# Optimization experiments

Hardware: AMD Instinct MI355X
Metric: run time of the kernel (lower is better)

## Reference

```python
import jax, jax.numpy as jnp
import numpy as np

N_NODES = 100000
N_EDGES = 1600000
N_GRAPHS = 128
K_HOPS = 3  # TAGConv default K
HIDDEN = 128
IN_FEAT = 4
NUM_CLASSES = 2


def setup_inputs() -> dict:
    key = jax.random.key(0)
    ks = jax.random.split(key, 10)
    x = jax.random.normal(ks[0], (N_NODES, IN_FEAT), dtype=jnp.float32)
    W1 = jax.random.normal(ks[1], (K_HOPS + 1, IN_FEAT, HIDDEN), dtype=jnp.float32) * 0.1
    b1 = jax.random.normal(ks[2], (HIDDEN,), dtype=jnp.float32) * 0.1
    W2 = jax.random.normal(ks[3], (K_HOPS + 1, HIDDEN, HIDDEN), dtype=jnp.float32) * 0.1
    b2 = jax.random.normal(ks[4], (HIDDEN,), dtype=jnp.float32) * 0.1
    Wlin = jax.random.normal(ks[5], (HIDDEN, NUM_CLASSES), dtype=jnp.float32) * 0.1
    blin = jax.random.normal(ks[6], (NUM_CLASSES,), dtype=jnp.float32) * 0.1
    edge_index = jax.random.randint(ks[7], (2, N_EDGES), 0, N_NODES, dtype=jnp.int32)
    batch = jnp.sort(jax.random.randint(ks[8], (N_NODES,), 0, N_GRAPHS, dtype=jnp.int32))
    return {"x": x, "W1": W1, "b1": b1, "W2": W2, "b2": b2,
            "Wlin": Wlin, "blin": blin, "edge_index": edge_index, "batch": batch}


def _gcn_norm(edge_index, num_nodes):
    # symmetric normalization, no self-loops (TAGConv: add_self_loops=False)
    row, col = edge_index[0], edge_index[1]
    ones = jnp.ones((edge_index.shape[1],), dtype=jnp.float32)
    deg = jax.ops.segment_sum(ones, col, num_segments=num_nodes)
    dinv = jnp.where(deg > 0, jax.lax.rsqrt(jnp.maximum(deg, 1.0)), 0.0)
    return dinv[row] * dinv[col]  # [E]


def _tagconv(x, row, col, norm, W, b):
    # out = sum_k (A_norm^k x) @ W[k] + b
    out = x @ W[0]
    h = x
    for k in range(1, W.shape[0]):
        h = jax.ops.segment_sum(h[row] * norm[:, None], col, num_segments=x.shape[0])
        out = out + h @ W[k]
    return out + b


def reference(x, W1, b1, W2, b2, Wlin, blin, edge_index, batch):
    row, col = edge_index[0], edge_index[1]
    norm = _gcn_norm(edge_index, x.shape[0])
    h = jax.nn.relu(_tagconv(x, row, col, norm, W1, b1))
    h = jax.nn.relu(_tagconv(h, row, col, norm, W2, b2))
    # global mean pool over graphs
    sums = jax.ops.segment_sum(h, batch, num_segments=N_GRAPHS)
    cnts = jax.ops.segment_sum(jnp.ones((h.shape[0],), dtype=h.dtype), batch, num_segments=N_GRAPHS)
    pooled = sums / jnp.maximum(cnts, 1.0)[:, None]
    # dropout is identity in eval mode
    logits = pooled @ Wlin + blin
    return jax.nn.softmax(logits, axis=-1)
```

## Files before the change

### kernel.cpp

```cpp
#include <hip/hip_runtime.h>

#define NNODES 100000
#define NEDGES 1600000
#define NGRAPHS 128
#define HID 128
#define NBKT 782
#define CHUNK 8192
#define NCHB ((NEDGES + CHUNK - 1) / CHUNK)
#define MAXB 3072

typedef unsigned short ushort_t;
typedef unsigned int uint_t;
typedef __attribute__((ext_vector_type(8))) short short8;
typedef __attribute__((ext_vector_type(4))) float floatx4;

__device__ __forceinline__ float bf2f(ushort_t u) {
    return __uint_as_float(((unsigned)u) << 16);
}
__device__ __forceinline__ ushort_t f2bf(float f) {
    unsigned u = __float_as_uint(f);
    return (ushort_t)((u + 0x7fffu + ((u >> 16) & 1u)) >> 16);
}

__global__ void hist_k(const int* __restrict__ col, int* __restrict__ bcnt) {
    __shared__ int l[NBKT];
    for (int i = threadIdx.x; i < NBKT; i += 256) l[i] = 0;
    __syncthreads();
    int base = blockIdx.x * CHUNK;
    int lim = base + CHUNK < NEDGES ? base + CHUNK : NEDGES;
    for (int e = base + threadIdx.x; e < lim; e += 256)
        atomicAdd(&l[col[e] >> 7], 1);
    __syncthreads();
    for (int i = threadIdx.x; i < NBKT; i += 256)
        if (l[i]) atomicAdd(&bcnt[i], l[i]);
}

__global__ void bscan_k(const int* __restrict__ bcnt, int* __restrict__ bbase,
                        int* __restrict__ gc) {
    __shared__ int l[1024];
    int t = threadIdx.x;
    int v0 = (t < NBKT) ? bcnt[t] : 0;
    l[t] = v0;
    __syncthreads();
    for (int d = 1; d < 1024; d <<= 1) {
        int v = (t >= d) ? l[t - d] : 0;
        __syncthreads();
        l[t] += v;
        __syncthreads();
    }
    if (t < NBKT) { int ex = l[t] - v0; bbase[t] = ex; gc[t] = ex; }
    if (t == 0) bbase[NBKT] = NEDGES;
}

__global__ void bfill_k(const int* __restrict__ row, const int* __restrict__ col,
                        int* __restrict__ gc, uint_t* __restrict__ entry) {
    __shared__ int lcnt[NBKT], lbase[NBKT];
    for (int i = threadIdx.x; i < NBKT; i += 256) lcnt[i] = 0;
    __syncthreads();
    int base = blockIdx.x * CHUNK;
    int lim = base + CHUNK < NEDGES ? base + CHUNK : NEDGES;
    for (int e = base + threadIdx.x; e < lim; e += 256)
        atomicAdd(&lcnt[col[e] >> 7], 1);
    __syncthreads();
    for (int i = threadIdx.x; i < NBKT; i += 256) {
        int c = lcnt[i];
        lbase[i] = c ? atomicAdd(&gc[i], c) : 0;
        lcnt[i] = 0;
    }
    __syncthreads();
    for (int e = base + threadIdx.x; e < lim; e += 256) {
        int c = col[e];
        int b = c >> 7;
        int pos = lbase[b] + atomicAdd(&lcnt[b], 1);
        entry[pos] = (uint_t)row[e] | ((uint_t)(c & 127) << 17);
    }
}

__global__ void sortb_k(const uint_t* __restrict__ entry, const int* __restrict__ bbase,
                        int* __restrict__ csr_src, int* __restrict__ degi,
                        int* __restrict__ off) {
    __shared__ uint_t ents[MAXB];
    __shared__ uint_t sorted[MAXB];
    __shared__ int ncnt[128], nsc[128], nfill[128];
    int b = blockIdx.x;
    int base = bbase[b];
    int cnt = bbase[b + 1] - base;
    if (cnt > MAXB) cnt = MAXB;
    int t = threadIdx.x;
    if (t < 128) { ncnt[t] = 0; nfill[t] = 0; }
    __syncthreads();
    for (int i = t; i < cnt; i += 256) {
        uint_t v = entry[base + i];
        ents[i] = v;
        atomicAdd(&ncnt[v >> 17], 1);
    }
    __syncthreads();
    if (t < 128) nsc[t] = ncnt[t];
    __syncthreads();
    for (int d = 1; d < 128; d <<= 1) {
        int v = (t >= d && t < 128) ? nsc[t - d] : 0;
        __syncthreads();
        if (t < 128) nsc[t] += v;
        __syncthreads();
    }
    if (t < 128) {
        int n = b * 128 + t;
        if (n < NNODES) { degi[n] = ncnt[t]; off[n] = base + nsc[t]; }
        nsc[t] -= ncnt[t];
    }
    __syncthreads();
    for (int i = t; i < cnt; i += 256) {
        uint_t v = ents[i];
        int dl = v >> 17;
        int pos = nsc[dl] + atomicAdd(&nfill[dl], 1);
        sorted[pos] = v & 0x1FFFFu;
    }
    __syncthreads();
    for (int i = t; i < cnt; i += 256) csr_src[base + i] = (int)sorted[i];
}

__global__ void dinv_kernel(const int* __restrict__ degi, float* __restrict__ dinv) {
    int i = blockIdx.x * blockDim.x + threadIdx.x;
    if (i < NNODES) {
        int d = degi[i];
        dinv[i] = (d > 0) ? rsqrtf((float)d) : 0.0f;
    }
}

__global__ void gprop4(const int* __restrict__ off, const int* __restrict__ csr_src,
                       const float* __restrict__ dinv,
                       const float* __restrict__ hin, float* __restrict__ hout) {
    int n = blockIdx.x * 256 + threadIdx.x;
    if (n >= NNODES) return;
    int k = n ? off[n - 1] : 0;
    int end = off[n];
    float dn = dinv[n];
    float4 acc = {0.f, 0.f, 0.f, 0.f};
    for (; k + 3 < end; k += 4) {
        int s0 = csr_src[k], s1 = csr_src[k + 1], s2 = csr_src[k + 2], s3 = csr_src[k + 3];
        float w0 = dinv[s0] * dn, w1 = dinv[s1] * dn, w2 = dinv[s2] * dn, w3 = dinv[s3] * dn;
        float4 v0 = *(const float4*)(hin + s0 * 4);
        float4 v1 = *(const float4*)(hin + s1 * 4);
        float4 v2 = *(const float4*)(hin + s2 * 4);
        float4 v3 = *(const float4*)(hin + s3 * 4);
        acc.x += w0 * v0.x + w1 * v1.x + w2 * v2.x + w3 * v3.x;
        acc.y += w0 * v0.y + w1 * v1.y + w2 * v2.y + w3 * v3.y;
        acc.z += w0 * v0.z + w1 * v1.z + w2 * v2.z + w3 * v3.z;
        acc.w += w0 * v0.w + w1 * v1.w + w2 * v2.w + w3 * v3.w;
    }
    for (; k < end; k++) {
        int s = csr_src[k];
        float w = dinv[s] * dn;
        float4 v = *(const float4*)(hin + s * 4);
        acc.x += w * v.x; acc.y += w * v.y; acc.z += w * v.z; acc.w += w * v.w;
    }
    *(float4*)(hout + n * 4) = acc;
}

__device__ __forceinline__ void acc8(float* a, float wgt, uint4 v) {
    a[0] += wgt * __uint_as_float(v.x << 16);
    a[1] += wgt * __uint_as_float(v.x & 0xffff0000u);
    a[2] += wgt * __uint_as_float(v.y << 16);
    a[3] += wgt * __uint_as_float(v.y & 0xffff0000u);
    a[4] += wgt * __uint_as_float(v.z << 16);
    a[5] += wgt * __uint_as_float(v.z & 0xffff0000u);
    a[6] += wgt * __uint_as_float(v.w << 16);
    a[7] += wgt * __uint_as_float(v.w & 0xffff0000u);
}

__global__ void gprop128(const int* __restrict__ off, const int* __restrict__ csr_src,
                         const float* __restrict__ dinv,
                         const ushort_t* __restrict__ hin, ushort_t* __restrict__ hout) {
    int t = blockIdx.x * 256 + threadIdx.x;
    int n = t >> 4, lane = t & 15;
    if (n >= NNODES) return;
    int k = n ? off[n - 1] : 0;
    int end = off[n];
    float dn = dinv[n];
    int fo = lane * 8;
    float a[8] = {0.f, 0.f, 0.f, 0.f, 0.f, 0.f, 0.f, 0.f};
    for (; k + 3 < end; k += 4) {
        int s0 = csr_src[k], s1 = csr_src[k + 1], s2 = csr_src[k + 2], s3 = csr_src[k + 3];
        float w0 = dinv[s0] * dn, w1 = dinv[s1] * dn, w2 = dinv[s2] * dn, w3 = dinv[s3] * dn;
        uint4 v0 = *(const uint4*)(hin + s0 * HID + fo);
        uint4 v1 = *(const uint4*)(hin + s1 * HID + fo);
        uint4 v2 = *(const uint4*)(hin + s2 * HID + fo);
        uint4 v3 = *(const uint4*)(hin + s3 * HID + fo);
        acc8(a, w0, v0); acc8(a, w1, v1); acc8(a, w2, v2); acc8(a, w3, v3);
    }
    for (; k < end; k++) {
        int s = csr_src[k];
        float w = dinv[s] * dn;
        uint4 v = *(const uint4*)(hin + s * HID + fo);
        acc8(a, w, v);
    }
    uint4 o;
    o.x = (unsigned)f2bf(a[0]) | ((unsigned)f2bf(a[1]) << 16);
    o.y = (unsigned)f2bf(a[2]) | ((unsigned)f2bf(a[3]) << 16);
    o.z = (unsigned)f2bf(a[4]) | ((unsigned)f2bf(a[5]) << 16);
    o.w = (unsigned)f2bf(a[6]) | ((unsigned)f2bf(a[7]) << 16);
    *(uint4*)(hout + n * HID + fo) = o;
}

__global__ void combine1(const float* __restrict__ x, const float* __restrict__ h1,
                         const float* __restrict__ h2, const float* __restrict__ h3,
                         const float* __restrict__ W1, const float* __restrict__ b1,
                         ushort_t* __restrict__ P0) {
    __shared__ float hs[4][16];
    int n0 = blockIdx.x * 4;
    int j = threadIdx.x;
    if (j < 64) {
        int n = j >> 4, v = j & 15, k = v >> 2, i = v & 3;
        const float* src = (k == 0) ? x : (k == 1) ? h1 : (k == 2) ? h2 : h3;
        hs[n][v] = src[(n0 + n) * 4 + i];
    }
    __syncthreads();
    float w[16];
#pragma unroll
    for (int v = 0; v < 16; v++) w[v] = W1[v * 128 + j];
    float bb = b1[j];
#pragma unroll
    for (int n = 0; n < 4; n++) {
        float acc = bb;
#pragma unroll
        for (int v = 0; v < 16; v++) acc += hs[n][v] * w[v];
        P0[(n0 + n) * 128 + j] = f2bf(fmaxf(acc, 0.0f));
    }
}

__global__ void wt_kernel(const float* __restrict__ W2, ushort_t* __restrict__ Wt) {
    int t = blockIdx.x * 256 + threadIdx.x;
    if (t >= 512 * 128) return;
    int j = t >> 9, k = t & 511;
    Wt[t] = f2bf(W2[k * 128 + j]);
}

__global__ __launch_bounds__(256) void gemm4p(
    const ushort_t* __restrict__ P0, const ushort_t* __restrict__ P1,
    const ushort_t* __restrict__ P2, const ushort_t* __restrict__ P3,
    const ushort_t* __restrict__ Wt, const float* __restrict__ b2,
    const int* __restrict__ batch, float* __restrict__ sums) {
    __shared__ ushort_t Bs[32768];
    int tid = threadIdx.x;
    int w = tid >> 6, lane = tid & 63;
    int r16 = lane & 15, kg = lane >> 4;
    int tb = blockIdx.x * 128 + w * 32;
    bool active = (tb < NNODES);
    floatx4 acc[2][8];
#pragma unroll
    for (int s = 0; s < 2; s++)
#pragma unroll
        for (int n = 0; n < 8; n++) acc[s][n] = (floatx4){0.f, 0.f, 0.f, 0.f};
    const ushort_t* Ps[4] = {P0, P1, P2, P3};
    for (int stage = 0; stage < 2; stage++) {
        __syncthreads();
#pragma unroll
        for (int i = 0; i < 16; i++) {
            int idx = i * 256 + tid;
            int r = idx >> 5;
            int slot = idx & 31;
            int cb = (slot * 16) ^ ((r & 7) << 4);
            *(uint4*)((char*)Bs + r * 512 + cb) =
                *(const uint4*)(Wt + r * 512 + stage * 256 + slot * 8);
        }
        __syncthreads();
        if (active) {
#pragma unroll
            for (int hh = 0; hh < 2; hh++) {
                const ushort_t* P = Ps[stage * 2 + hh];
#pragma unroll
                for (int k0 = 0; k0 < 128; k0 += 32) {
                    int f = k0 + kg * 8;
                    short8 a0 = *(const short8*)(P + (tb + r16) * HID + f);
                    short8 a1 = *(const short8*)(P + (tb + 16 + r16) * HID + f);
#pragma unroll
                    for (int n = 0; n < 8; n++) {
                        int r = n * 16 + r16;
                        int cb = (hh * 256 + k0 * 2 + kg * 16) ^ ((r & 7) << 4);
                        short8 b = *(const short8*)((const char*)Bs + r * 512 + cb);
                        acc[0][n] = __builtin_amdgcn_mfma_f32_16x16x32_bf16(a0, b, acc[0][n], 0, 0, 0);
                        acc[1][n] = __builtin_amdgcn_mfma_f32_16x16x32_bf16(a1, b, acc[1][n], 0, 0, 0);
                    }
                }
            }
        }
    }
    if (!active) return;
    float bb[8];
#pragma unroll
    for (int n = 0; n < 8; n++) bb[n] = b2[n * 16 + r16];
    int g0 = batch[tb], g31 = batch[tb + 31];
    if (g0 == g31) {
#pragma unroll
        for (int n = 0; n < 8; n++) {
            float s = 0.0f;
#pragma unroll
            for (int st = 0; st < 2; st++)
#pragma unroll
                for (int r = 0; r < 4; r++) s += fmaxf(acc[st][n][r] + bb[n], 0.0f);
            s += __shfl_xor(s, 16);
            s += __shfl_xor(s, 32);
            if (kg == 0) atomicAdd(&sums[g0 * HID + n * 16 + r16], s);
        }
    } else {
#pragma unroll
        for (int st = 0; st < 2; st++)
#pragma unroll
            for (int r = 0; r < 4; r++) {
                int g = batch[tb + st * 16 + kg * 4 + r];
#pragma unroll
                for (int n = 0; n < 8; n++)
                    atomicAdd(&sums[g * HID + n * 16 + r16], fmaxf(acc[st][n][r] + bb[n], 0.0f));
            }
    }
}

__global__ void bounds_kernel(const int* __restrict__ batch,
                              int* __restrict__ first, int* __restrict__ last) {
    int n = blockIdx.x * 256 + threadIdx.x;
    if (n >= NNODES) return;
    int g = batch[n];
    if (n == 0 || batch[n - 1] != g) first[g] = n;
    if (n == NNODES - 1 || batch[n + 1] != g) last[g] = n;
}

__global__ void head_kernel(const float* __restrict__ sums, const int* __restrict__ first,
                            const int* __restrict__ last,
                            const float* __restrict__ Wlin, const float* __restrict__ blin,
                            float* __restrict__ out) {
    int g = threadIdx.x;
    if (g >= NGRAPHS) return;
    int f = first[g];
    float cnt = (f >= 0) ? (float)(last[g] - f + 1) : 1.0f;
    float l0 = blin[0], l1 = blin[1];
    for (int i = 0; i < HID; i++) {
        float p = sums[g * HID + i] / cnt;
        l0 += p * Wlin[i * 2 + 0];
        l1 += p * Wlin[i * 2 + 1];
    }
    float m = fmaxf(l0, l1);
    float e0 = __expf(l0 - m), e1 = __expf(l1 - m);
    float s = e0 + e1;
    out[g * 2 + 0] = e0 / s;
    out[g * 2 + 1] = e1 / s;
}

#define NPAD      100096
#define OFF_DINV  0
#define OFF_DEGI  (OFF_DINV + NPAD)
#define OFF_OFF   (OFF_DEGI + NPAD)
#define OFF_BCNT  (OFF_OFF + NPAD)
#define OFF_BBASE (OFF_BCNT + 800)
#define OFF_GC    (OFF_BBASE + 800)
#define OFF_ENT   (OFF_GC + 800)
#define OFF_SRC   (OFF_ENT + NEDGES)
#define OFF_P0    (OFF_SRC + NEDGES)
#define OFF_P1    (OFF_P0 + NNODES * HID / 2)
#define OFF_P2    (OFF_P1 + NNODES * HID / 2)
#define OFF_P3    (OFF_P2 + NNODES * HID / 2)
#define OFF_H1    (OFF_P3 + NNODES * HID / 2)
#define OFF_H2    (OFF_H1 + NNODES * 4)
#define OFF_H3    (OFF_H2 + NNODES * 4)
#define OFF_WT    (OFF_H3 + NNODES * 4)
#define OFF_SUMS  (OFF_WT + 32768)
#define OFF_FIRST (OFF_SUMS + NGRAPHS * HID)
#define OFF_LAST  (OFF_FIRST + NGRAPHS)

extern "C" void kernel_launch(void* const* d_in, const int* in_sizes, int n_in,
                              void* d_out, int out_size, void* d_ws, size_t ws_size,
                              hipStream_t stream) {
    const float* x    = (const float*)d_in[0];
    const float* W1   = (const float*)d_in[1];
    const float* b1   = (const float*)d_in[2];
    const float* W2   = (const float*)d_in[3];
    const float* b2   = (const float*)d_in[4];
    const float* Wlin = (const float*)d_in[5];
    const float* blin = (const float*)d_in[6];
    const int* ei     = (const int*)d_in[7];
    const int* batch  = (const int*)d_in[8];
    float* out = (float*)d_out;

    const int* row = ei;
    const int* col = ei + NEDGES;

    float* ws = (float*)d_ws;
    float* dinv    = ws + OFF_DINV;
    int*   degi    = (int*)(ws + OFF_DEGI);
    int*   off     = (int*)(ws + OFF_OFF);
    int*   bcnt    = (int*)(ws + OFF_BCNT);
    int*   bbase   = (int*)(ws + OFF_BBASE);
    int*   gc      = (int*)(ws + OFF_GC);
    uint_t* ent    = (uint_t*)(ws + OFF_ENT);
    int*   csr_src = (int*)(ws + OFF_SRC);
    ushort_t* P0   = (ushort_t*)(ws + OFF_P0);
    ushort_t* P1   = (ushort_t*)(ws + OFF_P1);
    ushort_t* P2   = (ushort_t*)(ws + OFF_P2);
    ushort_t* P3   = (ushort_t*)(ws + OFF_P3);
    float* h1      = ws + OFF_H1;
    float* h2      = ws + OFF_H2;
    float* h3      = ws + OFF_H3;
    ushort_t* Wt   = (ushort_t*)(ws + OFF_WT);
    float* sums    = ws + OFF_SUMS;
    int*   first   = (int*)(ws + OFF_FIRST);
    int*   last    = (int*)(ws + OFF_LAST);

    hipMemsetAsync(bcnt, 0, 800 * sizeof(int), stream);
    hipMemsetAsync(sums, 0, NGRAPHS * HID * sizeof(float), stream);
    hipMemsetAsync(first, 0xFF, 2 * NGRAPHS * sizeof(int), stream);

    hist_k<<<NCHB, 256, 0, stream>>>(col, bcnt);
    bscan_k<<<1, 1024, 0, stream>>>(bcnt, bbase, gc);
    bfill_k<<<NCHB, 256, 0, stream>>>(row, col, gc, ent);
    sortb_k<<<NBKT, 256, 0, stream>>>(ent, bbase, csr_src, degi, off);
    dinv_kernel<<<(NNODES + 255) / 256, 256, 0, stream>>>(degi, dinv);
    wt_kernel<<<(512 * 128) / 256, 256, 0, stream>>>(W2, Wt);
    bounds_kernel<<<(NNODES + 255) / 256, 256, 0, stream>>>(batch, first, last);

    gprop4<<<(NNODES + 255) / 256, 256, 0, stream>>>(off, csr_src, dinv, x, h1);
    gprop4<<<(NNODES + 255) / 256, 256, 0, stream>>>(off, csr_src, dinv, h1, h2);
    gprop4<<<(NNODES + 255) / 256, 256, 0, stream>>>(off, csr_src, dinv, h2, h3);
    combine1<<<NNODES / 4, 128, 0, stream>>>(x, h1, h2, h3, W1, b1, P0);

    gprop128<<<(NNODES * 16) / 256, 256, 0, stream>>>(off, csr_src, dinv, P0, P1);
    gprop128<<<(NNODES * 16) / 256, 256, 0, stream>>>(off, csr_src, dinv, P1, P2);
    gprop128<<<(NNODES * 16) / 256, 256, 0, stream>>>(off, csr_src, dinv, P2, P3);

    gemm4p<<<(NNODES + 127) / 128, 256, 0, stream>>>(P0, P1, P2, P3, Wt, b2, batch, sums);

    head_kernel<<<1, 128, 0, stream>>>(sums, first, last, Wlin, blin, out);
}
```

Baseline: 360.1 us.

## Degree-sort nodes within buckets for balanced gathers and fuse setup kernels

The sort kernel now builds a per-bucket permutation that orders each 128-node bucket by in-degree (capped at 63). The gather propagation kernels process nodes in that order, so threads in the same wavefront handle nodes of similar degree, which is meant to cut divergence and idle lanes. The dinv, weight-transpose and graph-bounds kernels are merged into one launch, and the three memsets are merged into one contiguous zeroing. In exchange there is an extra indirection load per node, output writes become less sequential within a bucket, and the head now relies on zero-initialised first/last for empty graphs.

```diff
diff --git a/kernel.cpp b/kernel.cpp
--- a/kernel.cpp
+++ b/kernel.cpp
@@ -5,6 +5,7 @@
 #define NGRAPHS 128
 #define HID 128
 #define NBKT 782
+#define NPAD  (NBKT * 128)
 #define CHUNK 8192
 #define NCHB ((NEDGES + CHUNK - 1) / CHUNK)
 #define MAXB 3072
@@ -78,16 +79,18 @@
 
 __global__ void sortb_k(const uint_t* __restrict__ entry, const int* __restrict__ bbase,
                         int* __restrict__ csr_src, int* __restrict__ degi,
-                        int* __restrict__ off) {
+                        int* __restrict__ off, int* __restrict__ perm) {
     __shared__ uint_t ents[MAXB];
     __shared__ uint_t sorted[MAXB];
     __shared__ int ncnt[128], nsc[128], nfill[128];
+    __shared__ int dcnt[64], dbase_s[64], dfill[64];
     int b = blockIdx.x;
     int base = bbase[b];
     int cnt = bbase[b + 1] - base;
     if (cnt > MAXB) cnt = MAXB;
     int t = threadIdx.x;
     if (t < 128) { ncnt[t] = 0; nfill[t] = 0; }
+    if (t >= 128 && t < 192) { dcnt[t - 128] = 0; dfill[t - 128] = 0; }
     __syncthreads();
     for (int i = t; i < cnt; i += 256) {
         uint_t v = entry[base + i];
@@ -103,10 +106,13 @@
         if (t < 128) nsc[t] += v;
         __syncthreads();
     }
+    int mydeg = 0;
     if (t < 128) {
         int n = b * 128 + t;
         if (n < NNODES) { degi[n] = ncnt[t]; off[n] = base + nsc[t]; }
         nsc[t] -= ncnt[t];
+        mydeg = ncnt[t] > 63 ? 63 : ncnt[t];
+        atomicAdd(&dcnt[mydeg], 1);
     }
     __syncthreads();
     for (int i = t; i < cnt; i += 256) {
@@ -115,22 +121,42 @@
         int pos = nsc[dl] + atomicAdd(&nfill[dl], 1);
         sorted[pos] = v & 0x1FFFFu;
     }
-    __syncthreads();
+    if (t == 0) {
+        int run = 0;
+        for (int i = 0; i < 64; i++) { dbase_s[i] = run; run += dcnt[i]; }
+    }
+    __syncthreads();
+    if (t < 128) {
+        int pos = dbase_s[mydeg] + atomicAdd(&dfill[mydeg], 1);
+        perm[b * 128 + pos] = b * 128 + t;
+    }
     for (int i = t; i < cnt; i += 256) csr_src[base + i] = (int)sorted[i];
 }
 
-__global__ void dinv_kernel(const int* __restrict__ degi, float* __restrict__ dinv) {
-    int i = blockIdx.x * blockDim.x + threadIdx.x;
+__global__ void misc_k(const int* __restrict__ degi, float* __restrict__ dinv,
+                       const float* __restrict__ W2, ushort_t* __restrict__ Wt,
+                       const int* __restrict__ batch,
+                       int* __restrict__ first, int* __restrict__ last) {
+    int i = blockIdx.x * 256 + threadIdx.x;
     if (i < NNODES) {
         int d = degi[i];
         dinv[i] = (d > 0) ? rsqrtf((float)d) : 0.0f;
+        int g = batch[i];
+        if (i == 0 || batch[i - 1] != g) first[g] = i;
+        if (i == NNODES - 1 || batch[i + 1] != g) last[g] = i;
+    }
+    if (i < 512 * 128) {
+        int j = i >> 9, k = i & 511;
+        Wt[i] = f2bf(W2[k * 128 + j]);
     }
 }
 
 __global__ void gprop4(const int* __restrict__ off, const int* __restrict__ csr_src,
-                       const float* __restrict__ dinv,
+                       const float* __restrict__ dinv, const int* __restrict__ perm,
                        const float* __restrict__ hin, float* __restrict__ hout) {
-    int n = blockIdx.x * 256 + threadIdx.x;
+    int i = blockIdx.x * 256 + threadIdx.x;
+    if (i >= NPAD) return;
+    int n = perm[i];
     if (n >= NNODES) return;
     int k = n ? off[n - 1] : 0;
     int end = off[n];
@@ -169,10 +195,12 @@
 }
 
 __global__ void gprop128(const int* __restrict__ off, const int* __restrict__ csr_src,
-                         const float* __restrict__ dinv,
+                         const float* __restrict__ dinv, const int* __restrict__ perm,
                          const ushort_t* __restrict__ hin, ushort_t* __restrict__ hout) {
     int t = blockIdx.x * 256 + threadIdx.x;
-    int n = t >> 4, lane = t & 15;
+    int i = t >> 4, lane = t & 15;
+    if (i >= NPAD) return;
+    int n = perm[i];
     if (n >= NNODES) return;
     int k = n ? off[n - 1] : 0;
     int end = off[n];
@@ -228,13 +256,6 @@
     }
 }
 
-__global__ void wt_kernel(const float* __restrict__ W2, ushort_t* __restrict__ Wt) {
-    int t = blockIdx.x * 256 + threadIdx.x;
-    if (t >= 512 * 128) return;
-    int j = t >> 9, k = t & 511;
-    Wt[t] = f2bf(W2[k * 128 + j]);
-}
-
 __global__ __launch_bounds__(256) void gemm4p(
     const ushort_t* __restrict__ P0, const ushort_t* __restrict__ P1,
     const ushort_t* __restrict__ P2, const ushort_t* __restrict__ P3,
@@ -315,23 +336,14 @@
     }
 }
 
-__global__ void bounds_kernel(const int* __restrict__ batch,
-                              int* __restrict__ first, int* __restrict__ last) {
-    int n = blockIdx.x * 256 + threadIdx.x;
-    if (n >= NNODES) return;
-    int g = batch[n];
-    if (n == 0 || batch[n - 1] != g) first[g] = n;
-    if (n == NNODES - 1 || batch[n + 1] != g) last[g] = n;
-}
-
 __global__ void head_kernel(const float* __restrict__ sums, const int* __restrict__ first,
                             const int* __restrict__ last,
                             const float* __restrict__ Wlin, const float* __restrict__ blin,
                             float* __restrict__ out) {
     int g = threadIdx.x;
     if (g >= NGRAPHS) return;
-    int f = first[g];
-    float cnt = (f >= 0) ? (float)(last[g] - f + 1) : 1.0f;
+    float cnt = (float)(last[g] - first[g] + 1);
+    if (cnt < 1.0f) cnt = 1.0f;
     float l0 = blin[0], l1 = blin[1];
     for (int i = 0; i < HID; i++) {
         float p = sums[g * HID + i] / cnt;
@@ -345,11 +357,15 @@
     out[g * 2 + 1] = e1 / s;
 }
 
-#define NPAD      100096
 #define OFF_DINV  0
 #define OFF_DEGI  (OFF_DINV + NPAD)
 #define OFF_OFF   (OFF_DEGI + NPAD)
-#define OFF_BCNT  (OFF_OFF + NPAD)
+#define OFF_PERM  (OFF_OFF + NPAD)
+#define OFF_SUMS  (OFF_PERM + NPAD)
+#define OFF_FIRST (OFF_SUMS + NGRAPHS * HID)
+#define OFF_LAST  (OFF_FIRST + NGRAPHS)
+#define OFF_BCNT  (OFF_LAST + NGRAPHS)
+#define ZERO_WORDS (NGRAPHS * HID + NGRAPHS + NGRAPHS + 800)
 #define OFF_BBASE (OFF_BCNT + 800)
 #define OFF_GC    (OFF_BBASE + 800)
 #define OFF_ENT   (OFF_GC + 800)
@@ -362,9 +378,6 @@
 #define OFF_H2    (OFF_H1 + NNODES * 4)
 #define OFF_H3    (OFF_H2 + NNODES * 4)
 #define OFF_WT    (OFF_H3 + NNODES * 4)
-#define OFF_SUMS  (OFF_WT + 32768)
-#define OFF_FIRST (OFF_SUMS + NGRAPHS * HID)
-#define OFF_LAST  (OFF_FIRST + NGRAPHS)
 
 extern "C" void kernel_launch(void* const* d_in, const int* in_sizes, int n_in,
                               void* d_out, int out_size, void* d_ws, size_t ws_size,
@@ -387,6 +400,10 @@
     float* dinv    = ws + OFF_DINV;
     int*   degi    = (int*)(ws + OFF_DEGI);
     int*   off     = (int*)(ws + OFF_OFF);
+    int*   perm    = (int*)(ws + OFF_PERM);
+    float* sums    = ws + OFF_SUMS;
+    int*   first   = (int*)(ws + OFF_FIRST);
+    int*   last    = (int*)(ws + OFF_LAST);
     int*   bcnt    = (int*)(ws + OFF_BCNT);
     int*   bbase   = (int*)(ws + OFF_BBASE);
     int*   gc      = (int*)(ws + OFF_GC);
@@ -400,30 +417,23 @@
     float* h2      = ws + OFF_H2;
     float* h3      = ws + OFF_H3;
     ushort_t* Wt   = (ushort_t*)(ws + OFF_WT);
-    float* sums    = ws + OFF_SUMS;
-    int*   first   = (int*)(ws + OFF_FIRST);
-    int*   last    = (int*)(ws + OFF_LAST);
-
-    hipMemsetAsync(bcnt, 0, 800 * sizeof(int), stream);
-    hipMemsetAsync(sums, 0, NGRAPHS * HID * sizeof(float), stream);
-    hipMemsetAsync(first, 0xFF, 2 * NGRAPHS * sizeof(int), stream);
+
+    hipMemsetAsync(sums, 0, ZERO_WORDS * sizeof(float), stream);
 
     hist_k<<<NCHB, 256, 0, stream>>>(col, bcnt);
     bscan_k<<<1, 1024, 0, stream>>>(bcnt, bbase, gc);
     bfill_k<<<NCHB, 256, 0, stream>>>(row, col, gc, ent);
-    sortb_k<<<NBKT, 256, 0, stream>>>(ent, bbase, csr_src, degi, off);
-    dinv_kernel<<<(NNODES + 255) / 256, 256, 0, stream>>>(degi, dinv);
-    wt_kernel<<<(512 * 128) / 256, 256, 0, stream>>>(W2, Wt);
-    bounds_kernel<<<(NNODES + 255) / 256, 256, 0, stream>>>(batch, first, last);
-
-    gprop4<<<(NNODES + 255) / 256, 256, 0, stream>>>(off, csr_src, dinv, x, h1);
-    gprop4<<<(NNODES + 255) / 256, 256, 0, stream>>>(off, csr_src, dinv, h1, h2);
-    gprop4<<<(NNODES + 255) / 256, 256, 0, stream>>>(off, csr_src, dinv, h2, h3);
+    sortb_k<<<NBKT, 256, 0, stream>>>(ent, bbase, csr_src, degi, off, perm);
+    misc_k<<<(NPAD) / 256, 256, 0, stream>>>(degi, dinv, W2, Wt, batch, first, last);
+
+    gprop4<<<NPAD / 256, 256, 0, stream>>>(off, csr_src, dinv, perm, x, h1);
+    gprop4<<<NPAD / 256, 256, 0, stream>>>(off, csr_src, dinv, perm, h1, h2);
+    gprop4<<<NPAD / 256, 256, 0, stream>>>(off, csr_src, dinv, perm, h2, h3);
     combine1<<<NNODES / 4, 128, 0, stream>>>(x, h1, h2, h3, W1, b1, P0);
 
-    gprop128<<<(NNODES * 16) / 256, 256, 0, stream>>>(off, csr_src, dinv, P0, P1);
-    gprop128<<<(NNODES * 16) / 256, 256, 0, stream>>>(off, csr_src, dinv, P1, P2);
-    gprop128<<<(NNODES * 16) / 256, 256, 0, stream>>>(off, csr_src, dinv, P2, P3);
+    gprop128<<<NPAD * 16 / 256, 256, 0, stream>>>(off, csr_src, dinv, perm, P0, P1);
+    gprop128<<<NPAD * 16 / 256, 256, 0, stream>>>(off, csr_src, dinv, perm, P1, P2);
+    gprop128<<<NPAD * 16 / 256, 256, 0, stream>>>(off, csr_src, dinv, perm, P2, P3);
 
     gemm4p<<<(NNODES + 127) / 128, 256, 0, stream>>>(P0, P1, P2, P3, Wt, b2, batch, sums);
 
```

Result: slower. 402.3 us (+11.7%).
